# Optimization experiments

Hardware: AMD Instinct MI355X
Metric: run time of the kernel (lower is better)

Reference implementation:

```python
import jax, jax.numpy as jnp
import numpy as np
from jax import lax

N = 50000      # total nodes
E = 400000     # total edges
F = 512        # input feature dim
B = 50         # graphs in batch
NP = 1000      # nodes per graph
OUT = 10       # out_channel
EPS = 1e-5


def setup_inputs():
    key = jax.random.key(0)
    ks = jax.random.split(key, 20)
    x = jax.random.normal(ks[0], (N, F), jnp.float32)
    eg = jnp.arange(E) // (E // B)                       # graph id per edge
    src = jax.random.randint(ks[1], (E,), 0, NP) + eg * NP
    dst = jax.random.randint(ks[2], (E,), 0, NP) + eg * NP
    edge_index = jnp.stack([src, dst]).astype(jnp.int32)
    batch = (jnp.arange(N) // NP).astype(jnp.int32)
    s = 0.02
    W1 = s * jax.random.normal(ks[3], (1024, F), jnp.float32)
    b1 = jnp.zeros((1024,), jnp.float32)
    g1 = jnp.ones((1024,), jnp.float32)
    be1 = jnp.zeros((1024,), jnp.float32)
    Wp = s * jax.random.normal(ks[4], (1, 2 * 1024), jnp.float32)  # EdgePooling lin
    bp = jnp.zeros((1,), jnp.float32)
    W2 = s * jax.random.normal(ks[5], (512, 1024), jnp.float32)
    b2 = jnp.zeros((512,), jnp.float32)
    g2 = jnp.ones((512,), jnp.float32)
    be2 = jnp.zeros((512,), jnp.float32)
    Wfc = s * jax.random.normal(ks[6], (200, 512), jnp.float32)
    bfc = jnp.zeros((200,), jnp.float32)
    Wfc1 = s * jax.random.normal(ks[7], (OUT, 200), jnp.float32)
    bfc1 = jnp.zeros((OUT,), jnp.float32)
    return dict(x=x, edge_index=edge_index, batch=batch, W1=W1, b1=b1, g1=g1,
                be1=be1, Wp=Wp, bp=bp, W2=W2, b2=b2, g2=g2, be2=be2,
                Wfc=Wfc, bfc=bfc, Wfc1=Wfc1, bfc1=bfc1)


def _bn(h, g, b):
    m = h.mean(0)
    v = jnp.var(h, axis=0)  # biased var, as torch BatchNorm1d (train mode)
    return (h - m) * (g / jnp.sqrt(v + EPS)) + b


def _edge_pool(h, src, dst, batch, Wp, bp):
    # raw edge score: Linear([h_src || h_dst]) -> scalar per edge
    e = jnp.concatenate([h[src], h[dst]], axis=-1) @ Wp.T + bp  # [E,1]
    e = e[:, 0]
    # softmax over edges sharing the same destination node (PyG default)
    m = jax.ops.segment_max(e, dst, num_segments=N)
    ex = jnp.exp(e - m[dst])
    den = jax.ops.segment_sum(ex, dst, num_segments=N)
    score = ex / den[dst] + 0.5  # add_to_edge_score = 0.5

    # greedy contraction in descending-score order (sequential, like PyG)
    order = jnp.argsort(-score)
    so, do = src[order], dst[order]

    def step(merged, sd):
        s_, d_ = sd
        ok = (~merged[s_]) & (~merged[d_])
        merged = merged.at[s_].set(merged[s_] | ok)
        merged = merged.at[d_].set(merged[d_] | ok)
        return merged, ok

    _, valid = lax.scan(step, jnp.zeros(N, bool), (so, do))
    ec = (jnp.cumsum(valid.astype(jnp.int32)) - 1)      # cluster id per contracted edge
    num_merged = valid.astype(jnp.int32).sum()

    OOB = jnp.int32(N)
    cluster = jnp.full((N,), -1, jnp.int32)
    cluster = cluster.at[jnp.where(valid, so, OOB)].set(ec, mode='drop')
    cluster = cluster.at[jnp.where(valid, do, OOB)].set(ec, mode='drop')
    unmerged = cluster < 0
    rank = jnp.cumsum(unmerged.astype(jnp.int32)) - 1
    cluster = jnp.where(unmerged, num_merged + rank, cluster)

    # per-cluster multiplier: contracted-edge score, 1.0 for singleton nodes
    mult = jnp.ones((N,), h.dtype)
    mult = mult.at[jnp.where(valid, ec, OOB)].set(score[order], mode='drop')

    new_x = jax.ops.segment_sum(h, cluster, num_segments=N) * mult[:, None]
    new_batch = jnp.full((N,), B, jnp.int32).at[cluster].set(batch)  # pad slots -> dummy graph B
    return new_x, new_batch


def reference(x, edge_index, batch, W1, b1, g1, be1, Wp, bp, W2, b2, g2, be2,
              Wfc, bfc, Wfc1, bfc1):
    src, dst = edge_index[0], edge_index[1]
    # ChebConv K=1 == plain linear (only T_0 = x term)
    h = jax.nn.relu(_bn(x @ W1.T + b1, g1, be1))         # [N,1024]
    h, nb = _edge_pool(h, src, dst, batch, Wp, bp)       # [N,1024] padded, [N]
    h = jax.nn.relu(_bn(h @ W2.T + b2, g2, be2))         # [N,512]
    # global mean pool over graphs (dummy segment B holds padding)
    sums = jax.ops.segment_sum(h, nb, num_segments=B + 1)[:B]
    cnt = jax.ops.segment_sum(jnp.ones((N,), h.dtype), nb, num_segments=B + 1)[:B]
    pooled = sums / jnp.maximum(cnt, 1.0)[:, None]       # [B,512]
    hid = jax.nn.relu(pooled @ Wfc.T + bfc)              # [B,200]; dropout is eval no-op
    return hid @ Wfc1.T + bfc1                           # [B,OUT]
```

## Files before the change

kernel.cpp:

```cpp
#include <hip/hip_runtime.h>

#define Nn   50000
#define Ee   400000
#define Ff   512
#define H1   1024
#define H2   512
#define Bb   50
#define OUTd 10
#define EPSc 1e-5f
#define NPg  1000
#define EPg  8000

typedef _Float16 h8 __attribute__((ext_vector_type(8)));
typedef _Float16 h4 __attribute__((ext_vector_type(4)));
typedef float f4 __attribute__((ext_vector_type(4)));

__device__ __forceinline__ unsigned fmap(float f) {
    unsigned u = __float_as_uint(f);
    return (u & 0x80000000u) ? ~u : (u | 0x80000000u);
}
__device__ __forceinline__ float funmap(unsigned m) {
    unsigned u = (m & 0x80000000u) ? (m ^ 0x80000000u) : ~m;
    return __uint_as_float(u);
}

__device__ __forceinline__ void gl_lds16(const void* g, void* l) {
    __builtin_amdgcn_global_load_lds(
        (const __attribute__((address_space(1))) unsigned int*)g,
        (__attribute__((address_space(3))) unsigned int*)l,
        16, 0, 0);
}

__global__ void prep_kernel(const float* __restrict__ x, _Float16* __restrict__ xhi, _Float16* __restrict__ xlo,
                            const float* __restrict__ W1, _Float16* __restrict__ w1h, _Float16* __restrict__ w1l,
                            const float* __restrict__ W2, _Float16* __restrict__ w2h,
                            double* __restrict__ cs1, double* __restrict__ css1,
                            double* __restrict__ cs2, double* __restrict__ css2, int* __restrict__ scal) {
    int i = blockIdx.x * blockDim.x + threadIdx.x;
    int nth = gridDim.x * blockDim.x;
    for (int j = i; j < H1; j += nth) { cs1[j] = 0.0; css1[j] = 0.0; }
    for (int j = i; j < H2; j += nth) { cs2[j] = 0.0; css2[j] = 0.0; }
    if (i < 16) scal[i] = 0;
    const int nx = Nn * Ff / 4, nw1 = H1 * Ff / 4, nw2 = H2 * H1 / 4;
    for (int k = i; k < nx; k += nth) {
        float4 v = ((const float4*)x)[k];
        h4 H = { (_Float16)v.x, (_Float16)v.y, (_Float16)v.z, (_Float16)v.w };
        h4 L = { (_Float16)(v.x - (float)H[0]), (_Float16)(v.y - (float)H[1]),
                 (_Float16)(v.z - (float)H[2]), (_Float16)(v.w - (float)H[3]) };
        ((h4*)xhi)[k] = H;
        ((h4*)xlo)[k] = L;
    }
    for (int k = i; k < nw1; k += nth) {
        float4 v = ((const float4*)W1)[k];
        h4 H = { (_Float16)v.x, (_Float16)v.y, (_Float16)v.z, (_Float16)v.w };
        h4 L = { (_Float16)(v.x - (float)H[0]), (_Float16)(v.y - (float)H[1]),
                 (_Float16)(v.z - (float)H[2]), (_Float16)(v.w - (float)H[3]) };
        ((h4*)w1h)[k] = H;
        ((h4*)w1l)[k] = L;
    }
    for (int k = i; k < nw2; k += nth) {
        float4 v = ((const float4*)W2)[k];
        h4 H = { (_Float16)v.x, (_Float16)v.y, (_Float16)v.z, (_Float16)v.w };
        ((h4*)w2h)[k] = H;
    }
}

__global__ __launch_bounds__(512) void gemm1_256_kernel(
        const _Float16* __restrict__ Ahi, const _Float16* __restrict__ Alo,
        const _Float16* __restrict__ Bhi, const _Float16* __restrict__ Blo,
        const float* __restrict__ bias, float* __restrict__ C,
        double* __restrict__ csum, double* __restrict__ cssum)
{
    const int M = Nn;
    const int nwg = gridDim.x, orig = blockIdx.x;
    const int qq = nwg >> 3, rr = nwg & 7;
    const int xcd = orig & 7, idx = orig >> 3;
    const int lin = (xcd < rr ? xcd * (qq + 1) : rr * (qq + 1) + (xcd - rr) * qq) + idx;
    const int nT = H1 / 256;
    const int bmI = lin / nT;
    const int bm = bmI * 256, bn = (lin - bmI * nT) * 256;
    __shared__ __align__(16) _Float16 smem[2][4][256 * 32];
    const int tid = threadIdx.x, lane = tid & 63, wave = tid >> 6;
    const int rIn = lane >> 2;
    const int kSrcByte = ((((lane & 3) - ((lane >> 3) & 3)) & 3) << 4);
    const int wr = wave >> 2, wc = wave & 3;
    const int lr = lane & 15, kb = lane >> 4;
    const int pGr = ((kb + ((lr >> 1) & 3)) & 3) << 3;
    const int arr = wave >> 1;
    const int hv = wave & 1;
    const bool isA = (arr < 2);
    const _Float16* gp = (arr == 0) ? Ahi : (arr == 1) ? Alo : (arr == 2) ? Bhi : Blo;
    const int tb = isA ? bm : bn;
    f4 acc[8][4] = {};

    auto STAGE = [&](int b, int k0) {
        _Float16* lp = smem[b][arr] + hv * (128 * 32);
#pragma unroll
        for (int c = 0; c < 8; ++c) {
            int row = tb + hv * 128 + c * 16 + rIn;
            if (isA) row = min(row, M - 1);
            gl_lds16((const char*)gp + ((size_t)row * Ff + k0) * 2 + kSrcByte, lp + c * 512);
        }
    };

    int cur = 0;
    STAGE(0, 0);
    for (int k0 = 0; k0 < Ff; k0 += 32) {
        __syncthreads();
        if (k0 + 32 < Ff) STAGE(cur ^ 1, k0 + 32);
        const _Float16* AhP = smem[cur][0];
        const _Float16* AlP = smem[cur][1];
        const _Float16* BhP = smem[cur][2];
        const _Float16* BlP = smem[cur][3];
        h8 ahf[8], alf[8];
#pragma unroll
        for (int mi = 0; mi < 8; ++mi) {
            const int ar = (wr * 128 + mi * 16 + lr) * 32 + pGr;
            ahf[mi] = *(const h8*)&AhP[ar];
            alf[mi] = *(const h8*)&AlP[ar];
        }
#pragma unroll
        for (int ni = 0; ni < 4; ++ni) {
            const int br = (wc * 64 + ni * 16 + lr) * 32 + pGr;
            const h8 bh = *(const h8*)&BhP[br];
            const h8 bl = *(const h8*)&BlP[br];
#pragma unroll
            for (int mi = 0; mi < 8; ++mi) {
                acc[mi][ni] = __builtin_amdgcn_mfma_f32_16x16x32_f16(ahf[mi], bh, acc[mi][ni], 0, 0, 0);
                acc[mi][ni] = __builtin_amdgcn_mfma_f32_16x16x32_f16(ahf[mi], bl, acc[mi][ni], 0, 0, 0);
                acc[mi][ni] = __builtin_amdgcn_mfma_f32_16x16x32_f16(alf[mi], bh, acc[mi][ni], 0, 0, 0);
            }
        }
        cur ^= 1;
    }
#pragma unroll
    for (int ni = 0; ni < 4; ++ni) {
        const int col = bn + wc * 64 + ni * 16 + lr;
        const float bv = bias[col];
        double sd_ = 0.0, ssd = 0.0;
#pragma unroll
        for (int mi = 0; mi < 8; ++mi)
#pragma unroll
            for (int r = 0; r < 4; ++r) {
                int row = bm + wr * 128 + mi * 16 + kb * 4 + r;
                if (row < M) {
                    float v = acc[mi][ni][r] + bv;
                    C[(size_t)row * H1 + col] = v;
                    sd_ += (double)v;
                    ssd += (double)v * (double)v;
                }
            }
        sd_ += __shfl_xor(sd_, 16); ssd += __shfl_xor(ssd, 16);
        sd_ += __shfl_xor(sd_, 32); ssd += __shfl_xor(ssd, 32);
        if (kb == 0) {
            atomicAdd(&csum[col], sd_);
            atomicAdd(&cssum[col], ssd);
        }
    }
}

__global__ __launch_bounds__(256) void gemm2_kernel(
        const _Float16* __restrict__ Ag, const _Float16* __restrict__ Bh,
        const float* __restrict__ bias, float* __restrict__ C,
        const int* __restrict__ Mptr, int nT,
        double* __restrict__ csum, double* __restrict__ cssum)
{
    const int M = Mptr[0];
    const int nwg = gridDim.x, orig = blockIdx.x;
    const int qq = nwg >> 3, rr = nwg & 7;
    const int xcd = orig & 7, idx = orig >> 3;
    const int lin = (xcd < rr ? xcd * (qq + 1) : rr * (qq + 1) + (xcd - rr) * qq) + idx;
    const int bmI = lin / nT;
    const int bm = bmI * 128, bn = (lin - bmI * nT) * 128;
    if (bm >= M) return;
    __shared__ __align__(16) _Float16 smem[2][2][128 * 32];
    const int tid = threadIdx.x, lane = tid & 63, wave = tid >> 6;
    const int rIn = lane >> 2;
    const int kSrcByte = ((((lane & 3) - ((lane >> 3) & 3)) & 3) << 4);
    const int wr = wave >> 1, wc = wave & 1;
    const int lr = lane & 15, kb = lane >> 4;
    const int pGr = ((kb + ((lr >> 1) & 3)) & 3) << 3;
    f4 acc[4][4] = {};

    auto STAGE = [&](int b, int k0) {
        const bool isA = (wave < 2);
        const _Float16* gp = isA ? Ag : Bh;
        _Float16* lp = smem[b][isA ? 0 : 1];
        const int tb = isA ? bm : bn;
        const int hf = wave & 1;
#pragma unroll
        for (int c2 = 0; c2 < 4; ++c2) {
            int c = hf * 4 + c2;
            int row = tb + c * 16 + rIn;
            if (isA) row = min(row, M - 1);
            gl_lds16((const char*)gp + ((size_t)row * H1 + k0) * 2 + kSrcByte, lp + c * 512);
        }
    };

    int cur = 0;
    STAGE(0, 0);
    for (int k0 = 0; k0 < H1; k0 += 32) {
        __syncthreads();
        if (k0 + 32 < H1) STAGE(cur ^ 1, k0 + 32);
        const _Float16* AhP = smem[cur][0];
        const _Float16* BhP = smem[cur][1];
        const int ar = (wr * 64 + lr) * 32 + pGr;
        const int br = (wc * 64 + lr) * 32 + pGr;
        h8 ahf[4], bhf[4];
#pragma unroll
        for (int i = 0; i < 4; ++i) {
            ahf[i] = *(const h8*)&AhP[ar + i * 512];
            bhf[i] = *(const h8*)&BhP[br + i * 512];
        }
#pragma unroll
        for (int mi = 0; mi < 4; ++mi)
#pragma unroll
            for (int ni = 0; ni < 4; ++ni)
                acc[mi][ni] = __builtin_amdgcn_mfma_f32_16x16x32_f16(ahf[mi], bhf[ni], acc[mi][ni], 0, 0, 0);
        cur ^= 1;
    }
#pragma unroll
    for (int ni = 0; ni < 4; ++ni) {
        const int col = bn + wc * 64 + ni * 16 + lr;
        const float bv = bias[col];
        double sd_ = 0.0, ssd = 0.0;
#pragma unroll
        for (int mi = 0; mi < 4; ++mi)
#pragma unroll
            for (int r = 0; r < 4; ++r) {
                int row = bm + wr * 64 + mi * 16 + kb * 4 + r;
                if (row < M) {
                    float v = acc[mi][ni][r] + bv;
                    C[(size_t)row * H2 + col] = v;
                    sd_ += (double)v;
                    ssd += (double)v * (double)v;
                }
            }
        sd_ += __shfl_xor(sd_, 16); ssd += __shfl_xor(ssd, 16);
        sd_ += __shfl_xor(sd_, 32); ssd += __shfl_xor(ssd, 32);
        if (kb == 0) {
            atomicAdd(&csum[col], sd_);
            atomicAdd(&cssum[col], ssd);
        }
    }
}

__global__ void bnparam_kernel(const double* __restrict__ s, const double* __restrict__ ss,
                               const float* __restrict__ g, const float* __restrict__ be,
                               float* __restrict__ a, float* __restrict__ bb, int cols) {
    int j = blockIdx.x * blockDim.x + threadIdx.x;
    if (j >= cols) return;
    double sum = s[j], sumsq = ss[j];
    double mean = sum / (double)Nn;
    double var = sumsq / (double)Nn - mean * mean;
    float aj = g[j] / sqrtf((float)var + EPSc);
    a[j] = aj;
    bb[j] = be[j] - (float)mean * aj;
}

__global__ __launch_bounds__(256) void pq_kernel(const float* __restrict__ h,
        const float* __restrict__ a, const float* __restrict__ bb,
        const float* __restrict__ Wp, float* __restrict__ p, float* __restrict__ q) {
    const int n = blockIdx.x * 4 + (threadIdx.x >> 6);
    if (n >= Nn) return;
    const int lane = threadIdx.x & 63;
    float sp = 0.f, sq = 0.f;
    const float* row = h + (size_t)n * H1;
#pragma unroll
    for (int u = 0; u < 4; ++u) {
        int j = u * 256 + lane * 4;
        float4 v = *(const float4*)(row + j);
        const float4 av = *(const float4*)(a + j);
        const float4 bv = *(const float4*)(bb + j);
        v.x = fmaxf(v.x * av.x + bv.x, 0.f);
        v.y = fmaxf(v.y * av.y + bv.y, 0.f);
        v.z = fmaxf(v.z * av.z + bv.z, 0.f);
        v.w = fmaxf(v.w * av.w + bv.w, 0.f);
        const float4 wp = *(const float4*)(Wp + j);
        const float4 wq = *(const float4*)(Wp + H1 + j);
        sp += v.x * wp.x + v.y * wp.y + v.z * wp.z + v.w * wp.w;
        sq += v.x * wq.x + v.y * wq.y + v.z * wq.z + v.w * wq.w;
    }
#pragma unroll
    for (int off = 32; off > 0; off >>= 1) {
        sp += __shfl_xor(sp, off);
        sq += __shfl_xor(sq, off);
    }
    if (lane == 0) { p[n] = sp; q[n] = sq; }
}

__global__ __launch_bounds__(1024) void match_fused_kernel(
        const int* __restrict__ ei,
        const float* __restrict__ p, const float* __restrict__ q,
        const float* __restrict__ bp,
        unsigned long long* __restrict__ packed,
        int* __restrict__ nodeA, int* __restrict__ nodeB,
        float* __restrict__ multc, int* __restrict__ scal,
        int* __restrict__ gbase, int* __restrict__ gcnt) {
    __shared__ float earr[EPg];
    __shared__ float pl[NPg], ql[NPg];
    __shared__ unsigned maxu[NPg];
    __shared__ unsigned long long den[NPg];
    __shared__ unsigned short lst[2][EPg];
    __shared__ unsigned long long best[2][NPg];
    __shared__ int mergedS[NPg];
    __shared__ float lmult[NPg];
    __shared__ unsigned short lsA[NPg], ldA[NPg];
    __shared__ int cnts[4];

    const int g = blockIdx.x;
    const int tid = threadIdx.x;
    const int e0 = g * EPg, n0 = g * NPg;
    const int* srcp = ei + e0;
    const int* dstp = ei + Ee + e0;
    const float bpv = bp[0];

    for (int i = tid; i < NPg; i += 1024) {
        pl[i] = p[n0 + i];
        ql[i] = q[n0 + i];
        maxu[i] = 0u;
        den[i] = 0ull;
        best[0][i] = 0ull;
        mergedS[i] = 0;
    }
    __syncthreads();
    for (int i = tid; i < EPg; i += 1024) {
        int s = srcp[i] - n0, d = dstp[i] - n0;
        float e = pl[s] + ql[d] + bpv;
        earr[i] = e;
        atomicMax(&maxu[d], fmap(e));
    }
    __syncthreads();
    for (int i = tid; i < EPg; i += 1024) {
        int d = dstp[i] - n0;
        float ex = expf(earr[i] - funmap(maxu[d]));
        atomicAdd(&den[d], (unsigned long long)(ex * 4294967296.0f));
    }
    __syncthreads();
    for (int i = tid; i < EPg; i += 1024) {
        int s = srcp[i] - n0, d = dstp[i] - n0;
        float ex = expf(earr[i] - funmap(maxu[d]));
        float den_f = (float)((double)den[d] * (1.0 / 4294967296.0));
        float sc = ex / den_f + 0.5f;
        packed[e0 + i] = ((unsigned long long)__float_as_uint(sc) << 33)
                       | ((unsigned long long)(8191u - (unsigned)i) << 20)
                       | ((unsigned long long)(unsigned)s << 10) | (unsigned long long)(unsigned)d;
        lst[0][i] = (unsigned short)i;
    }
    if (tid == 0) { cnts[0] = EPg; cnts[1] = 0; cnts[2] = 0; }
    __syncthreads();
    int cur = 0, pb = 0;
    for (int round = 0; round < 20000; ++round) {
        const int n_cur = cnts[cur];
        if (n_cur == 0) break;
        if (tid == 0) cnts[cur ^ 1] = 0;
        for (int i = tid; i < NPg; i += 1024) best[pb ^ 1][i] = 0ull;
        for (int ii = tid; ii < n_cur; ii += 1024) {
            int le = lst[cur][ii];
            unsigned long long pk = packed[e0 + le];
            int s = (int)((pk >> 10) & 1023), d = (int)(pk & 1023);
            if (mergedS[s] | mergedS[d]) { lst[cur][ii] = 0xFFFF; continue; }
            atomicMax(&best[pb][s], pk);
            atomicMax(&best[pb][d], pk);
        }
        __syncthreads();
        for (int ii = tid; ii < n_cur; ii += 1024) {
            int le = lst[cur][ii];
            if (le == 0xFFFF) continue;
            unsigned long long pk = packed[e0 + le];
            int s = (int)((pk >> 10) & 1023), d = (int)(pk & 1023);
            if (best[pb][s] == pk && best[pb][d] == pk) {
                int c = atomicAdd(&cnts[2], 1);
                lsA[c] = (unsigned short)s;
                ldA[c] = (s == d) ? (unsigned short)0xFFFF : (unsigned short)d;
                lmult[c] = __uint_as_float((unsigned)(pk >> 33));
                mergedS[s] = 1;
                if (d != s) mergedS[d] = 1;
            } else {
                int pos = atomicAdd(&cnts[cur ^ 1], 1);
                lst[cur ^ 1][pos] = (unsigned short)le;
            }
        }
        __syncthreads();
        cur ^= 1;
        pb ^= 1;
    }
    for (int i = tid; i < NPg; i += 1024) {
        if (!mergedS[i]) {
            int c = atomicAdd(&cnts[2], 1);
            lsA[c] = (unsigned short)i;
            ldA[c] = 0xFFFF;
            lmult[c] = 1.0f;
        }
    }
    __syncthreads();
    if (tid == 0) {
        int ncl = cnts[2];
        int base = atomicAdd(&scal[2], ncl);
        cnts[3] = base;
        gbase[g] = base;
        gcnt[g] = ncl;
    }
    __syncthreads();
    const int ncl = cnts[2], base = cnts[3];
    for (int i = tid; i < ncl; i += 1024) {
        nodeA[base + i] = n0 + (int)lsA[i];
        nodeB[base + i] = (ldA[i] == 0xFFFF) ? -1 : (n0 + (int)ldA[i]);
        multc[base + i] = lmult[i];
    }
}

__global__ __launch_bounds__(256) void gather_kernel(const float* __restrict__ h,
        const float* __restrict__ a, const float* __restrict__ bb,
        const int* __restrict__ nodeA, const int* __restrict__ nodeB,
        const float* __restrict__ multc, const int* __restrict__ scal,
        _Float16* __restrict__ Ag) {
    int c = blockIdx.x * 4 + (threadIdx.x >> 6);
    if (c >= scal[2]) return;
    const int lane = threadIdx.x & 63;
    int na = nodeA[c], nb = nodeB[c];
    float mu = multc[c];
#pragma unroll
    for (int u = 0; u < 4; ++u) {
        int j = u * 256 + lane * 4;
        const float4 av = *(const float4*)(a + j);
        const float4 bv = *(const float4*)(bb + j);
        float4 v = *(const float4*)(h + (size_t)na * H1 + j);
        v.x = fmaxf(v.x * av.x + bv.x, 0.f);
        v.y = fmaxf(v.y * av.y + bv.y, 0.f);
        v.z = fmaxf(v.z * av.z + bv.z, 0.f);
        v.w = fmaxf(v.w * av.w + bv.w, 0.f);
        if (nb >= 0) {
            float4 w = *(const float4*)(h + (size_t)nb * H1 + j);
            v.x += fmaxf(w.x * av.x + bv.x, 0.f);
            v.y += fmaxf(w.y * av.y + bv.y, 0.f);
            v.z += fmaxf(w.z * av.z + bv.z, 0.f);
            v.w += fmaxf(w.w * av.w + bv.w, 0.f);
        }
        h4 o = { (_Float16)(mu * v.x), (_Float16)(mu * v.y), (_Float16)(mu * v.z), (_Float16)(mu * v.w) };
        *(h4*)(Ag + (size_t)c * H1 + j) = o;
    }
}

__global__ __launch_bounds__(256) void pool_seg_kernel(const float* __restrict__ C2,
        const double* __restrict__ cs2, const double* __restrict__ css2,
        const float* __restrict__ g2, const float* __restrict__ be2, const float* __restrict__ b2,
        const int* __restrict__ CvPtr,
        const int* __restrict__ gbase, const int* __restrict__ gcnt,
        float* __restrict__ pool) {
    const int g = blockIdx.x;
    const int j = blockIdx.y * 256 + threadIdx.x;
    double sum = cs2[j], sumsq = css2[j];
    double pad = (double)(Nn - CvPtr[0]);
    double bv = (double)b2[j];
    sum += pad * bv; sumsq += pad * bv * bv;
    double mean = sum / (double)Nn;
    double var = sumsq / (double)Nn - mean * mean;
    float aj = g2[j] / sqrtf((float)var + EPSc);
    float bj = be2[j] - (float)mean * aj;
    const int b0 = gbase[g], cN = gcnt[g];
    float s = 0.f;
    for (int c = b0; c < b0 + cN; ++c)
        s += fmaxf(C2[(size_t)c * H2 + j] * aj + bj, 0.f);
    pool[g * H2 + j] = s;
}

__global__ __launch_bounds__(256) void fc_kernel(const float* __restrict__ pool,
        const int* __restrict__ gcnt,
        const float* __restrict__ Wfc, const float* __restrict__ bfc,
        const float* __restrict__ Wfc1, const float* __restrict__ bfc1,
        float* __restrict__ out) {
    __shared__ float hidS[200];
    const int g = blockIdx.x;
    const int o = threadIdx.x;
    float inv = 1.0f / fmaxf((float)gcnt[g], 1.0f);
    if (o < 200) {
        float s = 0.f;
        for (int j = 0; j < H2; ++j) s += (pool[g * H2 + j] * inv) * Wfc[o * H2 + j];
        hidS[o] = fmaxf(s + bfc[o], 0.f);
    }
    __syncthreads();
    if (o < OUTd) {
        float s = bfc1[o];
        for (int t = 0; t < 200; ++t) s += hidS[t] * Wfc1[o * 200 + t];
        out[g * OUTd + o] = s;
    }
}

extern "C" void kernel_launch(void* const* d_in, const int* in_sizes, int n_in,
                              void* d_out, int out_size, void* d_ws, size_t ws_size,
                              hipStream_t stream) {
    (void)in_sizes; (void)n_in; (void)out_size; (void)ws_size;
    const float* x    = (const float*)d_in[0];
    const int*   ei   = (const int*)d_in[1];
    const float* W1   = (const float*)d_in[3];
    const float* b1   = (const float*)d_in[4];
    const float* g1   = (const float*)d_in[5];
    const float* be1  = (const float*)d_in[6];
    const float* Wp   = (const float*)d_in[7];
    const float* bp   = (const float*)d_in[8];
    const float* W2   = (const float*)d_in[9];
    const float* b2   = (const float*)d_in[10];
    const float* g2   = (const float*)d_in[11];
    const float* be2  = (const float*)d_in[12];
    const float* Wfc  = (const float*)d_in[13];
    const float* bfc  = (const float*)d_in[14];
    const float* Wfc1 = (const float*)d_in[15];
    const float* bfc1 = (const float*)d_in[16];

    char* w = (char*)d_ws;
    auto take = [&](size_t bytes) -> char* {
        char* r = w;
        w += (bytes + 255) & ~(size_t)255;
        return r;
    };
    float* h      = (float*)take((size_t)Nn * H1 * 4);
    _Float16* xhi = (_Float16*)take((size_t)Nn * Ff * 2);
    _Float16* xlo = (_Float16*)take((size_t)Nn * Ff * 2);
    _Float16* w1h = (_Float16*)take((size_t)H1 * Ff * 2);
    _Float16* w1l = (_Float16*)take((size_t)H1 * Ff * 2);
    _Float16* w2h = (_Float16*)take((size_t)H2 * H1 * 2);
    float* p      = (float*)take((size_t)Nn * 4);
    float* q      = (float*)take((size_t)Nn * 4);
    unsigned long long* packed = (unsigned long long*)take((size_t)Ee * 8);
    int* nodeA    = (int*)take((size_t)Nn * 4);
    int* nodeB    = (int*)take((size_t)Nn * 4);
    float* multc  = (float*)take((size_t)Nn * 4);
    double* cs1   = (double*)take((size_t)H1 * 8);
    double* css1  = (double*)take((size_t)H1 * 8);
    double* cs2   = (double*)take((size_t)H2 * 8);
    double* css2  = (double*)take((size_t)H2 * 8);
    float* a1     = (float*)take((size_t)H1 * 4);
    float* bb1    = (float*)take((size_t)H1 * 4);
    float* pool   = (float*)take((size_t)Bb * H2 * 4);
    int* scal     = (int*)take(64 * 4);
    int* gbase    = (int*)take(64 * 4);
    int* gcnt     = (int*)take(64 * 4);
    _Float16* Ag  = xhi;
    float* C2o    = h;

    const int mT  = (Nn + 127) / 128;
    const int mT2 = (Nn + 255) / 256;

    prep_kernel<<<dim3(2048), dim3(256), 0, stream>>>(x, xhi, xlo, W1, w1h, w1l, W2, w2h,
                                                      cs1, css1, cs2, css2, scal);
    gemm1_256_kernel<<<dim3(mT2 * (H1 / 256)), dim3(512), 0, stream>>>(
        xhi, xlo, w1h, w1l, b1, h, cs1, css1);
    bnparam_kernel<<<dim3((H1 + 255) / 256), dim3(256), 0, stream>>>(cs1, css1, g1, be1, a1, bb1, H1);
    pq_kernel<<<dim3((Nn + 3) / 4), dim3(256), 0, stream>>>(h, a1, bb1, Wp, p, q);
    match_fused_kernel<<<dim3(Bb), dim3(1024), 0, stream>>>(ei, p, q, bp, packed,
        nodeA, nodeB, multc, scal, gbase, gcnt);
    gather_kernel<<<dim3((Nn + 3) / 4), dim3(256), 0, stream>>>(h, a1, bb1, nodeA, nodeB, multc, scal, Ag);
    gemm2_kernel<<<dim3(mT * (H2 / 128)), dim3(256), 0, stream>>>(
        Ag, w2h, b2, C2o, scal + 2, H2 / 128, cs2, css2);
    pool_seg_kernel<<<dim3(Bb, H2 / 256), dim3(256), 0, stream>>>(
        C2o, cs2, css2, g2, be2, b2, scal + 2, gbase, gcnt, pool);
    fc_kernel<<<dim3(Bb), dim3(256), 0, stream>>>(pool, gcnt, Wfc, bfc, Wfc1, bfc1, (float*)d_out);
}
```

Baseline: 663.0 us.

## Split GEMM K-step into quadrant phases with interleaved staging and setprio

Restructures the first GEMM's main loop into four sub-phases per K step. Each phase loads a quarter of the fragments, issues a slice of the next-tile global-to-LDS copies, and runs its MFMAs at raised wave priority, with barriers between phases and an explicit vmcnt wait at the end. The goal is to spread memory traffic across the compute, cut the register pressure of holding all fragments at once, and make the waves on a CU interleave better. In exchange it adds more barriers per iteration and relies on manual scheduling choices.

```diff
diff --git a/kernel.cpp b/kernel.cpp
--- a/kernel.cpp
+++ b/kernel.cpp
@@ -93,45 +93,123 @@
     const int tb = isA ? bm : bn;
     f4 acc[8][4] = {};
 
-    auto STAGE = [&](int b, int k0) {
+    auto STAGE_RANGE = [&](int b, int k0, int c0, int c1) {
         _Float16* lp = smem[b][arr] + hv * (128 * 32);
-#pragma unroll
-        for (int c = 0; c < 8; ++c) {
+        for (int c = c0; c < c1; ++c) {
             int row = tb + hv * 128 + c * 16 + rIn;
             if (isA) row = min(row, M - 1);
             gl_lds16((const char*)gp + ((size_t)row * Ff + k0) * 2 + kSrcByte, lp + c * 512);
         }
     };
 
+    STAGE_RANGE(0, 0, 0, 8);
+    asm volatile("s_waitcnt vmcnt(0)" ::: "memory");
+    __builtin_amdgcn_sched_barrier(0);
+    __builtin_amdgcn_s_barrier();
+
     int cur = 0;
-    STAGE(0, 0);
-    for (int k0 = 0; k0 < Ff; k0 += 32) {
-        __syncthreads();
-        if (k0 + 32 < Ff) STAGE(cur ^ 1, k0 + 32);
+    for (int i = 0; i < Ff / 32; ++i) {
+        const int k0 = i * 32;
+        const bool more = (i + 1 < Ff / 32);
         const _Float16* AhP = smem[cur][0];
         const _Float16* AlP = smem[cur][1];
         const _Float16* BhP = smem[cur][2];
         const _Float16* BlP = smem[cur][3];
-        h8 ahf[8], alf[8];
-#pragma unroll
-        for (int mi = 0; mi < 8; ++mi) {
-            const int ar = (wr * 128 + mi * 16 + lr) * 32 + pGr;
-            ahf[mi] = *(const h8*)&AhP[ar];
-            alf[mi] = *(const h8*)&AlP[ar];
-        }
-#pragma unroll
-        for (int ni = 0; ni < 4; ++ni) {
-            const int br = (wc * 64 + ni * 16 + lr) * 32 + pGr;
-            const h8 bh = *(const h8*)&BhP[br];
-            const h8 bl = *(const h8*)&BlP[br];
-#pragma unroll
-            for (int mi = 0; mi < 8; ++mi) {
-                acc[mi][ni] = __builtin_amdgcn_mfma_f32_16x16x32_f16(ahf[mi], bh, acc[mi][ni], 0, 0, 0);
-                acc[mi][ni] = __builtin_amdgcn_mfma_f32_16x16x32_f16(ahf[mi], bl, acc[mi][ni], 0, 0, 0);
-                acc[mi][ni] = __builtin_amdgcn_mfma_f32_16x16x32_f16(alf[mi], bh, acc[mi][ni], 0, 0, 0);
+        h8 ah[4], al[4], bh[2], bl[2];
+
+#pragma unroll
+        for (int m2 = 0; m2 < 4; ++m2) {
+            const int ar_ = (wr * 128 + m2 * 16 + lr) * 32 + pGr;
+            ah[m2] = *(const h8*)&AhP[ar_];
+            al[m2] = *(const h8*)&AlP[ar_];
+        }
+#pragma unroll
+        for (int n2 = 0; n2 < 2; ++n2) {
+            const int br_ = (wc * 64 + n2 * 16 + lr) * 32 + pGr;
+            bh[n2] = *(const h8*)&BhP[br_];
+            bl[n2] = *(const h8*)&BlP[br_];
+        }
+        if (more) STAGE_RANGE(cur ^ 1, k0 + 32, 0, 2);
+        __builtin_amdgcn_s_setprio(1);
+#pragma unroll
+        for (int n2 = 0; n2 < 2; ++n2)
+#pragma unroll
+            for (int m2 = 0; m2 < 4; ++m2) {
+                acc[m2][n2] = __builtin_amdgcn_mfma_f32_16x16x32_f16(ah[m2], bh[n2], acc[m2][n2], 0, 0, 0);
+                acc[m2][n2] = __builtin_amdgcn_mfma_f32_16x16x32_f16(ah[m2], bl[n2], acc[m2][n2], 0, 0, 0);
+                acc[m2][n2] = __builtin_amdgcn_mfma_f32_16x16x32_f16(al[m2], bh[n2], acc[m2][n2], 0, 0, 0);
             }
-        }
-        cur ^= 1;
+        __builtin_amdgcn_s_setprio(0);
+        __builtin_amdgcn_s_barrier();
+
+#pragma unroll
+        for (int n2 = 0; n2 < 2; ++n2) {
+            const int br_ = (wc * 64 + (n2 + 2) * 16 + lr) * 32 + pGr;
+            bh[n2] = *(const h8*)&BhP[br_];
+            bl[n2] = *(const h8*)&BlP[br_];
+        }
+        if (more) STAGE_RANGE(cur ^ 1, k0 + 32, 2, 4);
+        __builtin_amdgcn_s_setprio(1);
+#pragma unroll
+        for (int n2 = 0; n2 < 2; ++n2)
+#pragma unroll
+            for (int m2 = 0; m2 < 4; ++m2) {
+                acc[m2][n2 + 2] = __builtin_amdgcn_mfma_f32_16x16x32_f16(ah[m2], bh[n2], acc[m2][n2 + 2], 0, 0, 0);
+                acc[m2][n2 + 2] = __builtin_amdgcn_mfma_f32_16x16x32_f16(ah[m2], bl[n2], acc[m2][n2 + 2], 0, 0, 0);
+                acc[m2][n2 + 2] = __builtin_amdgcn_mfma_f32_16x16x32_f16(al[m2], bh[n2], acc[m2][n2 + 2], 0, 0, 0);
+            }
+        __builtin_amdgcn_s_setprio(0);
+        __builtin_amdgcn_s_barrier();
+
+#pragma unroll
+        for (int m2 = 0; m2 < 4; ++m2) {
+            const int ar_ = (wr * 128 + (m2 + 4) * 16 + lr) * 32 + pGr;
+            ah[m2] = *(const h8*)&AhP[ar_];
+            al[m2] = *(const h8*)&AlP[ar_];
+        }
+#pragma unroll
+        for (int n2 = 0; n2 < 2; ++n2) {
+            const int br_ = (wc * 64 + n2 * 16 + lr) * 32 + pGr;
+            bh[n2] = *(const h8*)&BhP[br_];
+            bl[n2] = *(const h8*)&BlP[br_];
+        }
+        if (more) STAGE_RANGE(cur ^ 1, k0 + 32, 4, 6);
+        __builtin_amdgcn_s_setprio(1);
+#pragma unroll
+        for (int n2 = 0; n2 < 2; ++n2)
+#pragma unroll
+            for (int m2 = 0; m2 < 4; ++m2) {
+                acc[m2 + 4][n2] = __builtin_amdgcn_mfma_f32_16x16x32_f16(ah[m2], bh[n2], acc[m2 + 4][n2], 0, 0, 0);
+                acc[m2 + 4][n2] = __builtin_amdgcn_mfma_f32_16x16x32_f16(ah[m2], bl[n2], acc[m2 + 4][n2], 0, 0, 0);
+                acc[m2 + 4][n2] = __builtin_amdgcn_mfma_f32_16x16x32_f16(al[m2], bh[n2], acc[m2 + 4][n2], 0, 0, 0);
+            }
+        __builtin_amdgcn_s_setprio(0);
+        __builtin_amdgcn_s_barrier();
+
+#pragma unroll
+        for (int n2 = 0; n2 < 2; ++n2) {
+            const int br_ = (wc * 64 + (n2 + 2) * 16 + lr) * 32 + pGr;
+            bh[n2] = *(const h8*)&BhP[br_];
+            bl[n2] = *(const h8*)&BlP[br_];
+        }
+        if (more) STAGE_RANGE(cur ^ 1, k0 + 32, 6, 8);
+        __builtin_amdgcn_s_setprio(1);
+#pragma unroll
+        for (int n2 = 0; n2 < 2; ++n2)
+#pragma unroll
+            for (int m2 = 0; m2 < 4; ++m2) {
+                acc[m2 + 4][n2 + 2] = __builtin_amdgcn_mfma_f32_16x16x32_f16(ah[m2], bh[n2], acc[m2 + 4][n2 + 2], 0, 0, 0);
+                acc[m2 + 4][n2 + 2] = __builtin_amdgcn_mfma_f32_16x16x32_f16(ah[m2], bl[n2], acc[m2 + 4][n2 + 2], 0, 0, 0);
+                acc[m2 + 4][n2 + 2] = __builtin_amdgcn_mfma_f32_16x16x32_f16(al[m2], bh[n2], acc[m2 + 4][n2 + 2], 0, 0, 0);
+            }
+        __builtin_amdgcn_s_setprio(0);
+
+        if (more) {
+            asm volatile("s_waitcnt vmcnt(0)" ::: "memory");
+            __builtin_amdgcn_sched_barrier(0);
+            __builtin_amdgcn_s_barrier();
+            cur ^= 1;
+        }
     }
 #pragma unroll
     for (int ni = 0; ni < 4; ++ni) {
```

After: 663.2 us. About the same (+0.0%).
